# Optimization experiments

Measured on AMD Instinct MI355X. Metric: run time of the kernel, lower is better.

The kernel has to match this reference:

```python
import jax, jax.numpy as jnp
from jax import lax
import numpy as np

B, P, M1, M2, M3 = 128, 168, 2, 2, 2
M = M1 * M2 * M3
HIDC, HIDR, HIDS, CK, SKIP, HW = 50, 50, 5, 6, 24, 24
PT = (P - CK) // SKIP  # int((P-Ck)/skip) = 6
L = P - CK + 1         # 163


def gru(xs, w_ih, w_hh, b_ih, b_hh, hid):
    # xs: [T, N, in]; torch nn.GRU cell semantics, h0 = 0. Returns final h: [N, hid].
    def step(h, x):
        gi = x @ w_ih.T + b_ih
        gh = h @ w_hh.T + b_hh
        ir, iz, inn = jnp.split(gi, 3, axis=-1)
        hr, hz, hn = jnp.split(gh, 3, axis=-1)
        r = jax.nn.sigmoid(ir + hr)
        z = jax.nn.sigmoid(iz + hz)
        n = jnp.tanh(inn + r * hn)
        return (1.0 - z) * n + z * h, None
    h0 = jnp.zeros((xs.shape[1], hid), xs.dtype)
    h, _ = lax.scan(step, h0, xs)
    return h


def setup_inputs() -> dict:
    key = jax.random.key(0)
    ks = jax.random.split(key, 16)
    O = P * HIDC * CK  # 50400 conv output channels
    d = {
        'x': jax.random.normal(ks[0], (B, P, M1, M2, M3), jnp.float32),
        'conv_w': jax.random.normal(ks[1], (O, P, M1, M2, M3), jnp.float32) * 0.02,
        'conv_b': jax.random.normal(ks[2], (O,), jnp.float32) * 0.02,
        'g1_wih': jax.random.normal(ks[3], (3 * HIDR, HIDC), jnp.float32) * 0.1,
        'g1_whh': jax.random.normal(ks[4], (3 * HIDR, HIDR), jnp.float32) * 0.1,
        'g1_bih': jax.random.normal(ks[5], (3 * HIDR,), jnp.float32) * 0.1,
        'g1_bhh': jax.random.normal(ks[6], (3 * HIDR,), jnp.float32) * 0.1,
        'gs_wih': jax.random.normal(ks[7], (3 * HIDS, HIDC), jnp.float32) * 0.1,
        'gs_whh': jax.random.normal(ks[8], (3 * HIDS, HIDS), jnp.float32) * 0.1,
        'gs_bih': jax.random.normal(ks[9], (3 * HIDS,), jnp.float32) * 0.1,
        'gs_bhh': jax.random.normal(ks[10], (3 * HIDS,), jnp.float32) * 0.1,
        'l1_w': jax.random.normal(ks[11], (M, HIDR + SKIP * HIDS), jnp.float32) * 0.1,
        'l1_b': jax.random.normal(ks[12], (M,), jnp.float32) * 0.1,
        'hw_w': jax.random.normal(ks[13], (1, HW), jnp.float32) * 0.1,
        'hw_b': jax.random.normal(ks[14], (1,), jnp.float32) * 0.1,
    }
    return d


def reference(x, conv_w, conv_b, g1_wih, g1_whh, g1_bih, g1_bhh,
              gs_wih, gs_whh, gs_bih, gs_bhh, l1_w, l1_b, hw_w, hw_b):
    # Conv3d with kernel == full spatial extent is a dense matmul over (P*m1*m2*m3).
    xf = x.reshape(B, -1)                       # [B, P*M]
    wf = conv_w.reshape(conv_w.shape[0], -1)    # [O, P*M]
    c = jax.nn.relu(xf @ wf.T + conv_b)         # [B, O]
    c = c.reshape(B, HIDC, CK, P)
    # Diagonal strided sum (the torch triple loop): res1[b,c,t] = sum_k c[b,c,k,k+t]
    res1 = sum(c[:, :, k, k:k + L] for k in range(CK))  # [B, HIDC, L]
    # dropout: eval mode (identity)
    r = gru(jnp.transpose(res1, (2, 0, 1)), g1_wih, g1_whh, g1_bih, g1_bhh, HIDR)  # [B, HIDR]
    # skip GRU
    s = res1[:, :, -PT * SKIP:]                          # [B, HIDC, PT*SKIP]
    s = s.reshape(B, HIDC, PT, SKIP)
    s = jnp.transpose(s, (2, 0, 3, 1)).reshape(PT, B * SKIP, HIDC)
    hs = gru(s, gs_wih, gs_whh, gs_bih, gs_bhh, HIDS)    # [B*SKIP, HIDS]
    hs = hs.reshape(B, SKIP * HIDS)
    r = jnp.concatenate([r, hs], axis=1)                 # [B, HIDR + SKIP*HIDS]
    res = r @ l1_w.T + l1_b                              # [B, M]
    # highway (AR) component over the last HW timesteps
    z = x[:, -HW:].reshape(B, HW, M)                     # [B, HW, M]
    z = jnp.transpose(z, (0, 2, 1)).reshape(-1, HW)      # [B*M, HW]
    z = z @ hw_w.T + hw_b                                # [B*M, 1]
    res = res + z.reshape(B, M)
    res = jax.nn.sigmoid(res)
    return res.reshape(B, M1, M2, M3)
```

## Files before the change

kernel.cpp:

```cpp
#include <hip/hip_runtime.h>
#include <hip/hip_bf16.h>
#include <cstdint>


typedef __attribute__((ext_vector_type(8))) short short8;
typedef __attribute__((ext_vector_type(4))) float f32x4;

__device__ __forceinline__ unsigned short bf16rn(float f) {
    unsigned u = __float_as_uint(f);
    return (unsigned short)((u + 0x7FFFu + ((u >> 16) & 1u)) >> 16);
}
__device__ __forceinline__ unsigned pk2(float a, float b) {
    return ((unsigned)bf16rn(b) << 16) | (unsigned)bf16rn(a);
}
__device__ __forceinline__ uint4 pack8(float4 f0, float4 f1) {
    uint4 u;
    u.x = pk2(f0.x, f0.y); u.y = pk2(f0.z, f0.w);
    u.z = pk2(f1.x, f1.y); u.w = pk2(f1.z, f1.w);
    return u;
}
__device__ __forceinline__ float bf2f(unsigned short u) {
    return __uint_as_float((unsigned)u << 16);
}
__device__ __forceinline__ float sigmf(float x) { return 1.f / (1.f + __expf(-x)); }
__device__ __forceinline__ float tanhf_(float x) { return 1.f - 2.f / (__expf(2.f * x) + 1.f); }

__global__ __launch_bounds__(256, 2)
void k1_conv_gemm(const float* __restrict__ x, const float* __restrict__ w,
                  const float* __restrict__ bias, unsigned short* __restrict__ c) {
    __shared__ uint4 a_lds[8 * 129];
    __shared__ uint4 b_lds[8 * 113];
    const int tid  = threadIdx.x;
    const int n0   = blockIdx.x * 112;
    const int wave = tid >> 6, lane = tid & 63;
    const int quad = lane >> 4, m16 = lane & 15;

    f32x4 acc[2][7];
#pragma unroll
    for (int i = 0; i < 2; ++i)
#pragma unroll
        for (int j = 0; j < 7; ++j) acc[i][j] = (f32x4){0.f, 0.f, 0.f, 0.f};

    float4 pa[4][2];
    float4 pb[4][2];

    auto issue = [&](int kb) {
#pragma unroll
        for (int i = 0; i < 4; ++i) {
            int row = (tid >> 3) + 32 * i;
            const float* gp = x + row * 1344 + kb + (tid & 7) * 8;
            pa[i][0] = *reinterpret_cast<const float4*>(gp);
            pa[i][1] = *reinterpret_cast<const float4*>(gp + 4);
        }
#pragma unroll
        for (int i = 0; i < 4; ++i) {
            int idx = tid + 256 * i;
            if (idx < 896) {
                int row = idx >> 3;
                const float* gp = w + (size_t)(n0 + row) * 1344 + kb + (idx & 7) * 8;
                pb[i][0] = *reinterpret_cast<const float4*>(gp);
                pb[i][1] = *reinterpret_cast<const float4*>(gp + 4);
            }
        }
    };

    issue(0);
    for (int kb = 0; kb < 1344; kb += 64) {
#pragma unroll
        for (int i = 0; i < 4; ++i) {
            int idx = tid + 256 * i;
            int row = idx >> 3, ks = idx & 7;
            a_lds[ks * 129 + row] = pack8(pa[i][0], pa[i][1]);
        }
#pragma unroll
        for (int i = 0; i < 4; ++i) {
            int idx = tid + 256 * i;
            if (idx < 896) {
                int row = idx >> 3, ks = idx & 7;
                b_lds[ks * 113 + row] = pack8(pb[i][0], pb[i][1]);
            }
        }
        __syncthreads();
        if (kb + 64 < 1344) issue(kb + 64);
#pragma unroll
        for (int half = 0; half < 2; ++half) {
            const int kp = half * 4 + quad;
            short8 af[2], bfr[7];
#pragma unroll
            for (int rt = 0; rt < 2; ++rt)
                af[rt] = ((const short8*)a_lds)[kp * 129 + wave * 32 + rt * 16 + m16];
#pragma unroll
            for (int ct = 0; ct < 7; ++ct)
                bfr[ct] = ((const short8*)b_lds)[kp * 113 + ct * 16 + m16];
#pragma unroll
            for (int rt = 0; rt < 2; ++rt)
#pragma unroll
                for (int ct = 0; ct < 7; ++ct)
                    acc[rt][ct] = __builtin_amdgcn_mfma_f32_16x16x32_bf16(
                        af[rt], bfr[ct], acc[rt][ct], 0, 0, 0);
        }
        __syncthreads();
    }
#pragma unroll
    for (int ct = 0; ct < 7; ++ct) {
        int col = n0 + ct * 16 + m16;
        float bv = bias[col];
#pragma unroll
        for (int rt = 0; rt < 2; ++rt) {
#pragma unroll
            for (int r = 0; r < 4; ++r) {
                int grow = wave * 32 + rt * 16 + quad * 4 + r;
                float v = acc[rt][ct][r] + bv;
                v = fmaxf(v, 0.f);
                c[(size_t)grow * 50400 + col] = bf16rn(v);
            }
        }
    }
}

__global__ __launch_bounds__(256)
void k2f(const unsigned short* __restrict__ c,
         const float* __restrict__ g1_wih, const float* __restrict__ g1_bih,
         const float* __restrict__ gs_wih, const float* __restrict__ gs_bih,
         float* __restrict__ gi1, float* __restrict__ gi2) {
    __shared__ float xl[163 * 52];
    __shared__ float wl1[150 * 52];
    __shared__ float wl2[15 * 52];
    __shared__ float bl2[15];
    const int b = blockIdx.x;
    const int tid = threadIdx.x;
    const unsigned short* cb = c + (size_t)b * 50400;

    for (int i = tid; i < 7500; i += 256) {
        int r = i / 50, j = i - r * 50;
        wl1[r * 52 + j] = g1_wih[i];
    }
    for (int i = tid; i < 750; i += 256) {
        int r = i / 50, j = i - r * 50;
        wl2[r * 52 + j] = gs_wih[i];
    }
    if (tid < 15) bl2[tid] = gs_bih[tid];
    for (int idx = tid; idx < 8150; idx += 256) {
        int hc = idx / 163, t = idx - hc * 163;
        int base = hc * 1008 + t;
        float s = 0.f;
#pragma unroll
        for (int k = 0; k < 6; ++k) s += bf2f(cb[base + 169 * k]);
        xl[t * 52 + hc] = s;
    }
    __syncthreads();

    if (tid < 150) {
        const int cc = tid;
        float wr[50];
#pragma unroll
        for (int j = 0; j < 48; j += 4)
            *reinterpret_cast<float4*>(&wr[j]) =
                *reinterpret_cast<const float4*>(&wl1[cc * 52 + j]);
        wr[48] = wl1[cc * 52 + 48]; wr[49] = wl1[cc * 52 + 49];
        const float bv = g1_bih[cc];
        float* gout = gi1 + (size_t)b * 150 + cc;
        for (int t = 0; t < 163; ++t) {
            const float* xp = &xl[t * 52];
            float4 a = {0.f, 0.f, 0.f, 0.f};
#pragma unroll
            for (int j = 0; j < 48; j += 4) {
                float4 xv = *reinterpret_cast<const float4*>(xp + j);
                a.x += xv.x * wr[j + 0]; a.y += xv.y * wr[j + 1];
                a.z += xv.z * wr[j + 2]; a.w += xv.w * wr[j + 3];
            }
            float acc = bv + xp[48] * wr[48] + xp[49] * wr[49]
                      + (a.x + a.y) + (a.z + a.w);
            gout[(size_t)t * 128 * 150] = acc;
        }
    } else if (tid >= 192) {
        for (int e = tid - 192; e < 2160; e += 64) {
            int rr = e / 15, cc = e - rr * 15;
            int pt = rr / 24, sk = rr - pt * 24;
            int t = 19 + pt * 24 + sk;
            const float* xp = &xl[t * 52];
            const float* wp = &wl2[cc * 52];
            float4 a = {0.f, 0.f, 0.f, 0.f};
#pragma unroll
            for (int j = 0; j < 48; j += 4) {
                float4 xv = *reinterpret_cast<const float4*>(xp + j);
                float4 wv = *reinterpret_cast<const float4*>(wp + j);
                a.x += xv.x * wv.x; a.y += xv.y * wv.y;
                a.z += xv.z * wv.z; a.w += xv.w * wv.w;
            }
            float acc = bl2[cc] + xp[48] * wp[48] + xp[49] * wp[49]
                      + (a.x + a.y) + (a.z + a.w);
            gi2[(size_t)(pt * 3072 + b * 24 + sk) * 15 + cc] = acc;
        }
    }
}

__global__ __launch_bounds__(64)
void k4_gru1(const float* __restrict__ gi1, const float* __restrict__ whh,
             const float* __restrict__ bhh, float* __restrict__ r1) {
    __shared__ float wl[7500];
    __shared__ __align__(16) float hl[2][64];
    const int b = blockIdx.x;
    const int l = threadIdx.x;
    for (int idx = l; idx < 7500; idx += 64) wl[idx] = whh[idx];
    hl[0][l] = 0.f;
    hl[1][l] = 0.f;
    __syncthreads();
    const int lc = (l < 50) ? l : 49;
    float wr[50], wz[50], wn[50];
#pragma unroll
    for (int j = 0; j < 50; ++j) {
        wr[j] = wl[lc * 50 + j];
        wz[j] = wl[(50 + lc) * 50 + j];
        wn[j] = wl[(100 + lc) * 50 + j];
    }
    const float bhr = bhh[lc], bhz = bhh[50 + lc], bhn = bhh[100 + lc];
    float hcur = 0.f;
    const float* gp = gi1 + (size_t)b * 150;
    float gir = gp[lc], giz = gp[50 + lc], gin = gp[100 + lc];
    int p = 0;
    for (int t = 0; t < 163; ++t) {
        float ngir = 0.f, ngiz = 0.f, ngin = 0.f;
        if (t < 162) {
            const float* gq = gp + 150 * 128;
            ngir = gq[lc]; ngiz = gq[50 + lc]; ngin = gq[100 + lc];
        }
        const float* hp = hl[p];
        float ar = bhr, az = bhz, an = bhn;
#pragma unroll
        for (int j4 = 0; j4 < 12; ++j4) {
            float4 hv = *reinterpret_cast<const float4*>(hp + 4 * j4);
            ar += wr[4 * j4 + 0] * hv.x + wr[4 * j4 + 1] * hv.y +
                  wr[4 * j4 + 2] * hv.z + wr[4 * j4 + 3] * hv.w;
            az += wz[4 * j4 + 0] * hv.x + wz[4 * j4 + 1] * hv.y +
                  wz[4 * j4 + 2] * hv.z + wz[4 * j4 + 3] * hv.w;
            an += wn[4 * j4 + 0] * hv.x + wn[4 * j4 + 1] * hv.y +
                  wn[4 * j4 + 2] * hv.z + wn[4 * j4 + 3] * hv.w;
        }
        {
            float h48 = hp[48], h49 = hp[49];
            ar += wr[48] * h48 + wr[49] * h49;
            az += wz[48] * h48 + wz[49] * h49;
            an += wn[48] * h48 + wn[49] * h49;
        }
        float rg = sigmf(gir + ar);
        float zg = sigmf(giz + az);
        float ng = tanhf_(gin + rg * an);
        float hn = (1.f - zg) * ng + zg * hcur;
        hl[1 - p][l] = hn;
        __syncthreads();
        p ^= 1;
        hcur = hn;
        gir = ngir; giz = ngiz; gin = ngin;
        gp += 150 * 128;
    }
    if (l < 50) r1[b * 50 + l] = hcur;
}

__global__ __launch_bounds__(256)
void k5_gru2(const float* __restrict__ gi2, const float* __restrict__ whh,
             const float* __restrict__ bhh, float* __restrict__ hs) {
    __shared__ float wl[75];
    __shared__ float bl[15];
    const int tid = threadIdx.x;
    if (tid < 75) wl[tid] = whh[tid];
    if (tid < 15) bl[tid] = bhh[tid];
    __syncthreads();
    const int bsk = blockIdx.x * 256 + tid;
    float h[5] = {0.f, 0.f, 0.f, 0.f, 0.f};
    for (int pt = 0; pt < 6; ++pt) {
        const float* gp = gi2 + (size_t)(pt * 3072 + bsk) * 15;
        float gi[15];
#pragma unroll
        for (int i = 0; i < 15; ++i) gi[i] = gp[i];
        float gh[15];
#pragma unroll
        for (int i = 0; i < 15; ++i) {
            float s = bl[i];
#pragma unroll
            for (int j = 0; j < 5; ++j) s += wl[i * 5 + j] * h[j];
            gh[i] = s;
        }
#pragma unroll
        for (int u = 0; u < 5; ++u) {
            float rg = sigmf(gi[u] + gh[u]);
            float zg = sigmf(gi[5 + u] + gh[5 + u]);
            float ng = tanhf_(gi[10 + u] + rg * gh[10 + u]);
            h[u] = (1.f - zg) * ng + zg * h[u];
        }
    }
#pragma unroll
    for (int u = 0; u < 5; ++u) hs[bsk * 5 + u] = h[u];
}

__global__ __launch_bounds__(256)
void k6_final(const float* __restrict__ r1, const float* __restrict__ hs,
              const float* __restrict__ l1w, const float* __restrict__ l1b,
              const float* __restrict__ x, const float* __restrict__ hww,
              const float* __restrict__ hwb, float* __restrict__ out) {
    const int tid = blockIdx.x * 256 + threadIdx.x;
    if (tid >= 1024) return;
    const int b = tid >> 3, m = tid & 7;
    float acc = l1b[m];
    const float* wrow = l1w + m * 170;
    const float* rb = r1 + b * 50;
#pragma unroll
    for (int j = 0; j < 50; ++j) acc += rb[j] * wrow[j];
    const float* hb = hs + b * 120;
#pragma unroll
    for (int j = 0; j < 120; ++j) acc += hb[j] * wrow[50 + j];
    float z = hwb[0];
    const float* xb = x + b * 1344 + 144 * 8 + m;
#pragma unroll
    for (int wi = 0; wi < 24; ++wi) z += xb[wi * 8] * hww[wi];
    out[tid] = 1.f / (1.f + __expf(-(acc + z)));
}

extern "C" void kernel_launch(void* const* d_in, const int* in_sizes, int n_in,
                              void* d_out, int out_size, void* d_ws, size_t ws_size,
                              hipStream_t stream) {
    const float* x      = (const float*)d_in[0];
    const float* conv_w = (const float*)d_in[1];
    const float* conv_b = (const float*)d_in[2];
    const float* g1_wih = (const float*)d_in[3];
    const float* g1_whh = (const float*)d_in[4];
    const float* g1_bih = (const float*)d_in[5];
    const float* g1_bhh = (const float*)d_in[6];
    const float* gs_wih = (const float*)d_in[7];
    const float* gs_whh = (const float*)d_in[8];
    const float* gs_bih = (const float*)d_in[9];
    const float* gs_bhh = (const float*)d_in[10];
    const float* l1_w   = (const float*)d_in[11];
    const float* l1_b   = (const float*)d_in[12];
    const float* hw_w   = (const float*)d_in[13];
    const float* hw_b   = (const float*)d_in[14];
    float* out = (float*)d_out;

    char* ws = (char*)d_ws;
    unsigned short* c   = (unsigned short*)(ws);
    float* gi1          = (float*)(ws + 12902400);
    float* gi2          = (float*)(ws + 25420800);
    float* r1           = (float*)(ws + 26526720);
    float* hs           = (float*)(ws + 26552320);

    hipLaunchKernelGGL(k1_conv_gemm, dim3(450), dim3(256), 0, stream, x, conv_w, conv_b, c);
    hipLaunchKernelGGL(k2f,          dim3(128), dim3(256), 0, stream, c, g1_wih, g1_bih,
                       gs_wih, gs_bih, gi1, gi2);
    hipLaunchKernelGGL(k4_gru1,      dim3(128), dim3(64),  0, stream, gi1, g1_whh, g1_bhh, r1);
    hipLaunchKernelGGL(k5_gru2,      dim3(12),  dim3(256), 0, stream, gi2, gs_whh, gs_bhh, hs);
    hipLaunchKernelGGL(k6_final,     dim3(4),   dim3(256), 0, stream, r1, hs, l1_w, l1_b, x, hw_w, hw_b, out);
}
```

Baseline: 592.8 us.

## Shrink conv GEMM N-tile, pre-convert x to bf16, fuse skip GRU and output

The conv GEMM N-tile drops from 112 to 48 columns, so 1050 blocks run instead of 450, with occupancy raised to 4 blocks per CU to spread the weight stream across more CUs. A new k0_cvt kernel converts x to bf16 once, so GEMM blocks load packed A tiles directly and skip per-tile conversion. The skip GRU and final linear/highway/sigmoid stage are folded into the tail of the main GRU kernel, removing two launches and the intermediate buffers. The cost is more redundant A-tile loading across the extra blocks and one extra small launch.

```diff
diff --git a/kernel.cpp b/kernel.cpp
--- a/kernel.cpp
+++ b/kernel.cpp
@@ -25,84 +25,85 @@
 __device__ __forceinline__ float sigmf(float x) { return 1.f / (1.f + __expf(-x)); }
 __device__ __forceinline__ float tanhf_(float x) { return 1.f - 2.f / (__expf(2.f * x) + 1.f); }
 
-__global__ __launch_bounds__(256, 2)
-void k1_conv_gemm(const float* __restrict__ x, const float* __restrict__ w,
+__global__ __launch_bounds__(256)
+void k0_cvt(const float* __restrict__ x, unsigned short* __restrict__ xb) {
+    int i = (blockIdx.x * 256 + threadIdx.x) * 8;
+    float4 f0 = *reinterpret_cast<const float4*>(x + i);
+    float4 f1 = *reinterpret_cast<const float4*>(x + i + 4);
+    *reinterpret_cast<uint4*>(xb + i) = pack8(f0, f1);
+}
+
+__global__ __launch_bounds__(256, 4)
+void k1_conv_gemm(const unsigned short* __restrict__ xb, const float* __restrict__ w,
                   const float* __restrict__ bias, unsigned short* __restrict__ c) {
     __shared__ uint4 a_lds[8 * 129];
-    __shared__ uint4 b_lds[8 * 113];
+    __shared__ uint4 b_lds[8 * 49];
     const int tid  = threadIdx.x;
-    const int n0   = blockIdx.x * 112;
+    const int n0   = blockIdx.x * 48;
     const int wave = tid >> 6, lane = tid & 63;
     const int quad = lane >> 4, m16 = lane & 15;
 
-    f32x4 acc[2][7];
+    f32x4 acc[2][3];
 #pragma unroll
     for (int i = 0; i < 2; ++i)
 #pragma unroll
-        for (int j = 0; j < 7; ++j) acc[i][j] = (f32x4){0.f, 0.f, 0.f, 0.f};
-
-    float4 pa[4][2];
-    float4 pb[4][2];
+        for (int j = 0; j < 3; ++j) acc[i][j] = (f32x4){0.f, 0.f, 0.f, 0.f};
+
+    const int arow = tid >> 3, aks = tid & 7;
+    const int brow1 = (tid + 256) >> 3;
+
+    uint4  pa[4];
+    float4 pb0[2], pb1[2];
 
     auto issue = [&](int kb) {
 #pragma unroll
         for (int i = 0; i < 4; ++i) {
-            int row = (tid >> 3) + 32 * i;
-            const float* gp = x + row * 1344 + kb + (tid & 7) * 8;
-            pa[i][0] = *reinterpret_cast<const float4*>(gp);
-            pa[i][1] = *reinterpret_cast<const float4*>(gp + 4);
-        }
-#pragma unroll
-        for (int i = 0; i < 4; ++i) {
-            int idx = tid + 256 * i;
-            if (idx < 896) {
-                int row = idx >> 3;
-                const float* gp = w + (size_t)(n0 + row) * 1344 + kb + (idx & 7) * 8;
-                pb[i][0] = *reinterpret_cast<const float4*>(gp);
-                pb[i][1] = *reinterpret_cast<const float4*>(gp + 4);
-            }
+            const unsigned short* gp = xb + (arow + 32 * i) * 1344 + kb + aks * 8;
+            pa[i] = *reinterpret_cast<const uint4*>(gp);
+        }
+        {
+            const float* gp = w + (size_t)(n0 + arow) * 1344 + kb + aks * 8;
+            pb0[0] = *reinterpret_cast<const float4*>(gp);
+            pb0[1] = *reinterpret_cast<const float4*>(gp + 4);
+        }
+        if (tid < 128) {
+            const float* gp = w + (size_t)(n0 + brow1) * 1344 + kb + aks * 8;
+            pb1[0] = *reinterpret_cast<const float4*>(gp);
+            pb1[1] = *reinterpret_cast<const float4*>(gp + 4);
         }
     };
 
     issue(0);
     for (int kb = 0; kb < 1344; kb += 64) {
 #pragma unroll
-        for (int i = 0; i < 4; ++i) {
-            int idx = tid + 256 * i;
-            int row = idx >> 3, ks = idx & 7;
-            a_lds[ks * 129 + row] = pack8(pa[i][0], pa[i][1]);
-        }
-#pragma unroll
-        for (int i = 0; i < 4; ++i) {
-            int idx = tid + 256 * i;
-            if (idx < 896) {
-                int row = idx >> 3, ks = idx & 7;
-                b_lds[ks * 113 + row] = pack8(pb[i][0], pb[i][1]);
-            }
-        }
+        for (int i = 0; i < 4; ++i)
+            a_lds[aks * 129 + arow + 32 * i] = pa[i];
+        b_lds[aks * 49 + arow] = pack8(pb0[0], pb0[1]);
+        if (tid < 128)
+            b_lds[aks * 49 + brow1] = pack8(pb1[0], pb1[1]);
         __syncthreads();
         if (kb + 64 < 1344) issue(kb + 64);
 #pragma unroll
         for (int half = 0; half < 2; ++half) {
             const int kp = half * 4 + quad;
-            short8 af[2], bfr[7];
+            short8 af[2], bfr[3];
 #pragma unroll
             for (int rt = 0; rt < 2; ++rt)
                 af[rt] = ((const short8*)a_lds)[kp * 129 + wave * 32 + rt * 16 + m16];
 #pragma unroll
-            for (int ct = 0; ct < 7; ++ct)
-                bfr[ct] = ((const short8*)b_lds)[kp * 113 + ct * 16 + m16];
+            for (int ct = 0; ct < 3; ++ct)
+                bfr[ct] = ((const short8*)b_lds)[kp * 49 + ct * 16 + m16];
 #pragma unroll
             for (int rt = 0; rt < 2; ++rt)
 #pragma unroll
-                for (int ct = 0; ct < 7; ++ct)
+                for (int ct = 0; ct < 3; ++ct)
                     acc[rt][ct] = __builtin_amdgcn_mfma_f32_16x16x32_bf16(
                         af[rt], bfr[ct], acc[rt][ct], 0, 0, 0);
         }
         __syncthreads();
     }
 #pragma unroll
-    for (int ct = 0; ct < 7; ++ct) {
+    for (int ct = 0; ct < 3; ++ct) {
         int col = n0 + ct * 16 + m16;
         float bv = bias[col];
 #pragma unroll
@@ -197,12 +198,19 @@
 
 __global__ __launch_bounds__(64)
 void k4_gru1(const float* __restrict__ gi1, const float* __restrict__ whh,
-             const float* __restrict__ bhh, float* __restrict__ r1) {
+             const float* __restrict__ bhh, const float* __restrict__ gi2,
+             const float* __restrict__ gs_whh, const float* __restrict__ gs_bhh,
+             const float* __restrict__ l1w, const float* __restrict__ l1b,
+             const float* __restrict__ x, const float* __restrict__ hww,
+             const float* __restrict__ hwb, float* __restrict__ out) {
     __shared__ float wl[7500];
+    __shared__ float g2[90];
     __shared__ __align__(16) float hl[2][64];
     const int b = blockIdx.x;
     const int l = threadIdx.x;
     for (int idx = l; idx < 7500; idx += 64) wl[idx] = whh[idx];
+    for (int i = l; i < 75; i += 64) g2[i] = gs_whh[i];
+    if (l < 15) g2[75 + l] = gs_bhh[l];
     hl[0][l] = 0.f;
     hl[1][l] = 0.f;
     __syncthreads();
@@ -254,66 +262,49 @@
         gir = ngir; giz = ngiz; gin = ngin;
         gp += 150 * 128;
     }
-    if (l < 50) r1[b * 50 + l] = hcur;
-}
-
-__global__ __launch_bounds__(256)
-void k5_gru2(const float* __restrict__ gi2, const float* __restrict__ whh,
-             const float* __restrict__ bhh, float* __restrict__ hs) {
-    __shared__ float wl[75];
-    __shared__ float bl[15];
-    const int tid = threadIdx.x;
-    if (tid < 75) wl[tid] = whh[tid];
-    if (tid < 15) bl[tid] = bhh[tid];
+    if (l < 50) wl[l] = hcur;
     __syncthreads();
-    const int bsk = blockIdx.x * 256 + tid;
-    float h[5] = {0.f, 0.f, 0.f, 0.f, 0.f};
-    for (int pt = 0; pt < 6; ++pt) {
-        const float* gp = gi2 + (size_t)(pt * 3072 + bsk) * 15;
-        float gi[15];
-#pragma unroll
-        for (int i = 0; i < 15; ++i) gi[i] = gp[i];
-        float gh[15];
-#pragma unroll
-        for (int i = 0; i < 15; ++i) {
-            float s = bl[i];
-#pragma unroll
-            for (int j = 0; j < 5; ++j) s += wl[i * 5 + j] * h[j];
-            gh[i] = s;
-        }
-#pragma unroll
-        for (int u = 0; u < 5; ++u) {
-            float rg = sigmf(gi[u] + gh[u]);
-            float zg = sigmf(gi[5 + u] + gh[5 + u]);
-            float ng = tanhf_(gi[10 + u] + rg * gh[10 + u]);
-            h[u] = (1.f - zg) * ng + zg * h[u];
-        }
-    }
-#pragma unroll
-    for (int u = 0; u < 5; ++u) hs[bsk * 5 + u] = h[u];
-}
-
-__global__ __launch_bounds__(256)
-void k6_final(const float* __restrict__ r1, const float* __restrict__ hs,
-              const float* __restrict__ l1w, const float* __restrict__ l1b,
-              const float* __restrict__ x, const float* __restrict__ hww,
-              const float* __restrict__ hwb, float* __restrict__ out) {
-    const int tid = blockIdx.x * 256 + threadIdx.x;
-    if (tid >= 1024) return;
-    const int b = tid >> 3, m = tid & 7;
-    float acc = l1b[m];
-    const float* wrow = l1w + m * 170;
-    const float* rb = r1 + b * 50;
-#pragma unroll
-    for (int j = 0; j < 50; ++j) acc += rb[j] * wrow[j];
-    const float* hb = hs + b * 120;
-#pragma unroll
-    for (int j = 0; j < 120; ++j) acc += hb[j] * wrow[50 + j];
-    float z = hwb[0];
-    const float* xb = x + b * 1344 + 144 * 8 + m;
-#pragma unroll
-    for (int wi = 0; wi < 24; ++wi) z += xb[wi * 8] * hww[wi];
-    out[tid] = 1.f / (1.f + __expf(-(acc + z)));
+    if (l < 24) {
+        float h[5] = {0.f, 0.f, 0.f, 0.f, 0.f};
+        for (int pt = 0; pt < 6; ++pt) {
+            const float* gq = gi2 + (size_t)(pt * 3072 + b * 24 + l) * 15;
+            float gi[15];
+#pragma unroll
+            for (int i = 0; i < 15; ++i) gi[i] = gq[i];
+            float gh[15];
+#pragma unroll
+            for (int i = 0; i < 15; ++i) {
+                float s = g2[75 + i];
+#pragma unroll
+                for (int j = 0; j < 5; ++j) s += g2[i * 5 + j] * h[j];
+                gh[i] = s;
+            }
+#pragma unroll
+            for (int u = 0; u < 5; ++u) {
+                float rg = sigmf(gi[u] + gh[u]);
+                float zg = sigmf(gi[5 + u] + gh[5 + u]);
+                float ng = tanhf_(gi[10 + u] + rg * gh[10 + u]);
+                h[u] = (1.f - zg) * ng + zg * h[u];
+            }
+        }
+#pragma unroll
+        for (int u = 0; u < 5; ++u) wl[64 + l * 5 + u] = h[u];
+    }
+    __syncthreads();
+    if (l < 8) {
+        const int m = l;
+        float acc = l1b[m];
+        const float* wrow = l1w + m * 170;
+#pragma unroll
+        for (int j = 0; j < 50; ++j) acc += wl[j] * wrow[j];
+#pragma unroll
+        for (int j = 0; j < 120; ++j) acc += wl[64 + j] * wrow[50 + j];
+        float z = hwb[0];
+        const float* xb2 = x + b * 1344 + 1152 + m;
+#pragma unroll
+        for (int wi = 0; wi < 24; ++wi) z += xb2[wi * 8] * hww[wi];
+        out[b * 8 + m] = sigmf(acc + z);
+    }
 }
 
 extern "C" void kernel_launch(void* const* d_in, const int* in_sizes, int n_in,
@@ -340,13 +331,12 @@
     unsigned short* c   = (unsigned short*)(ws);
     float* gi1          = (float*)(ws + 12902400);
     float* gi2          = (float*)(ws + 25420800);
-    float* r1           = (float*)(ws + 26526720);
-    float* hs           = (float*)(ws + 26552320);
-
-    hipLaunchKernelGGL(k1_conv_gemm, dim3(450), dim3(256), 0, stream, x, conv_w, conv_b, c);
-    hipLaunchKernelGGL(k2f,          dim3(128), dim3(256), 0, stream, c, g1_wih, g1_bih,
+    unsigned short* xbf = (unsigned short*)(ws + 26526720);
+
+    hipLaunchKernelGGL(k0_cvt,       dim3(84),   dim3(256), 0, stream, x, xbf);
+    hipLaunchKernelGGL(k1_conv_gemm, dim3(1050), dim3(256), 0, stream, xbf, conv_w, conv_b, c);
+    hipLaunchKernelGGL(k2f,          dim3(128),  dim3(256), 0, stream, c, g1_wih, g1_bih,
                        gs_wih, gs_bih, gi1, gi2);
-    hipLaunchKernelGGL(k4_gru1,      dim3(128), dim3(64),  0, stream, gi1, g1_whh, g1_bhh, r1);
-    hipLaunchKernelGGL(k5_gru2,      dim3(12),  dim3(256), 0, stream, gi2, gs_whh, gs_bhh, hs);
-    hipLaunchKernelGGL(k6_final,     dim3(4),   dim3(256), 0, stream, r1, hs, l1_w, l1_b, x, hw_w, hw_b, out);
-}
+    hipLaunchKernelGGL(k4_gru1,      dim3(128),  dim3(64),  0, stream, gi1, g1_whh, g1_bhh,
+                       gi2, gs_whh, gs_bhh, l1_w, l1_b, x, hw_w, hw_b, out);
+}
```

Measured after the change: 698.9 us. 1.18x slower.
